# Performance work log

Hardware: AMD Instinct MI355X
Metric: run time of the kernel (lower is better)

The kernel has to match this reference:

```python
import jax, jax.numpy as jnp
import numpy as np

HEADS = 8
GROUPS = 8  # min(8, ch)
EPS = 1e-5


def group_norm(x, gamma, beta):
    # x: (B, C, H, W); normalize over (C/G, H, W) per group
    B, C, H, W = x.shape
    xg = x.reshape(B, GROUPS, C // GROUPS, H, W)
    mu = jnp.mean(xg, axis=(2, 3, 4), keepdims=True)
    var = jnp.var(xg, axis=(2, 3, 4), keepdims=True)
    xn = ((xg - mu) * jax.lax.rsqrt(var + EPS)).reshape(B, C, H, W)
    return xn * gamma[None, :, None, None] + beta[None, :, None, None]


def setup_inputs() -> dict:
    key = jax.random.key(0)
    k1, k2, k3 = jax.random.split(key, 3)
    B, C, H, W = 8, 512, 32, 32
    x = jax.random.normal(k1, (B, C, H, W), dtype=jnp.float32)
    gn_gamma = jnp.ones((C,), dtype=jnp.float32)
    gn_beta = jnp.zeros((C,), dtype=jnp.float32)
    # conv1x1 weights, torch shape (out,in,1,1) squeezed to (out,in)
    w_qkv = jax.random.normal(k2, (3 * C, C), dtype=jnp.float32) * (1.0 / np.sqrt(C))
    w_proj = jax.random.normal(k3, (C, C), dtype=jnp.float32) * (1.0 / np.sqrt(C))
    b_proj = jnp.zeros((C,), dtype=jnp.float32)
    return {"x": x, "gn_gamma": gn_gamma, "gn_beta": gn_beta,
            "w_qkv": w_qkv, "w_proj": w_proj, "b_proj": b_proj}


def reference(x, gn_gamma, gn_beta, w_qkv, w_proj, b_proj):
    B, C, H, W = x.shape
    hd = C // HEADS  # head_dim
    N = H * W
    xn = group_norm(x, gn_gamma, gn_beta)
    # 1x1 conv == channel matmul: (B,3C,H,W)
    qkv = jnp.einsum('oc,bchw->bohw', w_qkv, xn)
    q, k, v = jnp.split(qkv, 3, axis=1)

    def sh(t):  # (B,C,H,W) -> (B, heads, N, head_dim)
        return t.reshape(B, HEADS, hd, N).transpose(0, 1, 3, 2)

    q, k, v = sh(q), sh(k), sh(v)
    scale = hd ** -0.5
    attn = jax.nn.softmax(jnp.einsum('bhnd,bhmd->bhnm', q, k) * scale, axis=-1)
    out = jnp.einsum('bhnm,bhmd->bhnd', attn, v)  # (B,heads,N,hd)
    out = out.transpose(0, 1, 3, 2).reshape(B, C, H, W)
    proj = jnp.einsum('oc,bchw->bohw', w_proj, out) + b_proj[None, :, None, None]
    return x + proj
```

## Files before the change

kernel.cpp:

```cpp
#include <hip/hip_runtime.h>
#include <cstdint>


typedef __bf16 bf16_t;
typedef bf16_t bf16x8 __attribute__((ext_vector_type(8)));
typedef float f32x4 __attribute__((ext_vector_type(4)));

__device__ __forceinline__ uint16_t f2bf(float f) {
  uint32_t x = __builtin_bit_cast(uint32_t, f);
  x += 0x7FFFu + ((x >> 16) & 1u);
  return (uint16_t)(x >> 16);
}
__device__ __forceinline__ bf16x8 frag_ld(const uint16_t* p) {
  return __builtin_bit_cast(bf16x8, *(const uint4*)p);
}
__device__ __forceinline__ void gl_lds16(const uint16_t* g, uint16_t* l) {
  __builtin_amdgcn_global_load_lds(
      (const __attribute__((address_space(1))) uint32_t*)g,
      (__attribute__((address_space(3))) uint32_t*)l, 16, 0, 0);
}
#define MFMA16(a, b, c) __builtin_amdgcn_mfma_f32_16x16x32_bf16((a), (b), (c), 0, 0, 0)

__global__ __launch_bounds__(256) void prep_k(const float* __restrict__ wq,
                                              const float* __restrict__ wp,
                                              uint16_t* __restrict__ wqb,
                                              uint16_t* __restrict__ wpb,
                                              const float* __restrict__ x,
                                              float* __restrict__ stats) {
  __shared__ alignas(16) float r1[256];
  __shared__ alignas(16) float r2[256];
  int bx = blockIdx.x, t = threadIdx.x;
  if (bx < 512) {
    int idx = (bx * 256 + t) * 8;
    const float* s;
    uint16_t* d;
    if (idx < 786432) { s = wq + idx; d = wqb + idx; }
    else              { s = wp + (idx - 786432); d = wpb + (idx - 786432); }
    float4 a = *(const float4*)s;
    float4 b = *(const float4*)(s + 4);
    union { uint16_t u[8]; uint4 v; } o;
    o.u[0] = f2bf(a.x); o.u[1] = f2bf(a.y); o.u[2] = f2bf(a.z); o.u[3] = f2bf(a.w);
    o.u[4] = f2bf(b.x); o.u[5] = f2bf(b.y); o.u[6] = f2bf(b.z); o.u[7] = f2bf(b.w);
    *(uint4*)d = o.v;
    return;
  }
  int pg = bx - 512;
  const float4* p4 = (const float4*)(x + (size_t)(pg >> 2) * 65536 + (pg & 3) * 16384);
  float s1 = 0.f, s2 = 0.f;
  for (int i = t; i < 4096; i += 256) {
    float4 u = p4[i];
    s1 += u.x + u.y + u.z + u.w;
    s2 += u.x * u.x + u.y * u.y + u.z * u.z + u.w * u.w;
  }
  r1[t] = s1; r2[t] = s2; __syncthreads();
  for (int o = 128; o > 0; o >>= 1) {
    if (t < o) { r1[t] += r1[t + o]; r2[t] += r2[t + o]; }
    __syncthreads();
  }
  if (t == 0) { stats[pg * 2] = r1[0]; stats[pg * 2 + 1] = r2[0]; }
}

__global__ __launch_bounds__(256) void gn_apply_k(const float* __restrict__ x,
                                                  const float* __restrict__ gamma,
                                                  const float* __restrict__ beta,
                                                  const float* __restrict__ stats,
                                                  uint16_t* __restrict__ xn) {
  int nt = blockIdx.x, g = blockIdx.y, b = blockIdx.z;
  int n0 = nt * 64;
  int bg = b * 8 + g;
  float s1 = 0.f, s2 = 0.f;
#pragma unroll
  for (int p = 0; p < 4; p++) { s1 += stats[(bg * 4 + p) * 2]; s2 += stats[(bg * 4 + p) * 2 + 1]; }
  float mu   = s1 * (1.0f / 65536.0f);
  float var  = s2 * (1.0f / 65536.0f) - mu * mu;
  float rstd = rsqrtf(var + 1e-5f);
  __shared__ alignas(16) uint16_t tile[64][72];
  int t = threadIdx.x;
  {
    int c_loc = t >> 2;
    int nch = (t & 3) * 16;
    int c = g * 64 + c_loc;
    float gm = gamma[c], bt = beta[c];
    const float* src = x + (size_t)b * 524288 + (size_t)c * 1024 + n0 + nch;
#pragma unroll
    for (int hh = 0; hh < 2; hh++) {
      float4 u0 = *(const float4*)(src + hh * 8);
      float4 u1 = *(const float4*)(src + hh * 8 + 4);
      union { uint16_t u16[8]; uint4 v; } o;
      o.u16[0] = f2bf((u0.x - mu) * rstd * gm + bt);
      o.u16[1] = f2bf((u0.y - mu) * rstd * gm + bt);
      o.u16[2] = f2bf((u0.z - mu) * rstd * gm + bt);
      o.u16[3] = f2bf((u0.w - mu) * rstd * gm + bt);
      o.u16[4] = f2bf((u1.x - mu) * rstd * gm + bt);
      o.u16[5] = f2bf((u1.y - mu) * rstd * gm + bt);
      o.u16[6] = f2bf((u1.z - mu) * rstd * gm + bt);
      o.u16[7] = f2bf((u1.w - mu) * rstd * gm + bt);
      *(uint4*)&tile[c_loc][nch + hh * 8] = o.v;
    }
  }
  __syncthreads();
  {
    int n_loc = t >> 2;
    int c0 = (t & 3) * 16;
    union { uint16_t u16[16]; uint4 v[2]; } o;
#pragma unroll
    for (int j = 0; j < 16; j++) o.u16[j] = tile[c0 + j][n_loc];
    uint16_t* dst = xn + (size_t)b * 524288 + (size_t)(n0 + n_loc) * 512 + g * 64 + c0;
    *(uint4*)dst = o.v[0];
    *(uint4*)(dst + 8) = o.v[1];
  }
}

template <int MODE>
__device__ __forceinline__ void gemm_body(uint16_t* Sh,
                                          const uint16_t* Arow, const uint16_t* Brow,
                                          uint16_t* O0, uint16_t* O1,
                                          int b, int n0, int o0) {
  uint16_t* As = Sh;
  uint16_t* Bs = Sh + 8192;
  int t = threadIdx.x;
  int lane = t & 63, w = t >> 6;
  int qd = lane >> 4, l15 = lane & 15;
  int wm = w & 1, wn = w >> 1;

  const uint16_t* gA[4];
  const uint16_t* gB[4];
  uint16_t* lA[4];
  uint16_t* lB[4];
#pragma unroll
  for (int i = 0; i < 4; i++) {
    int p = i * 256 + t;
    int row = p >> 3, slot = p & 7, gc = slot ^ (row & 7);
    gA[i] = Arow + (size_t)row * 512 + gc * 8;
    gB[i] = Brow + (size_t)row * 512 + gc * 8;
    lA[i] = As + (size_t)(p - lane) * 8;
    lB[i] = Bs + (size_t)(p - lane) * 8;
  }

  f32x4 acc[4][4] = {};

  for (int k0 = 0; k0 < 512; k0 += 64) {
    __syncthreads();
#pragma unroll
    for (int i = 0; i < 4; i++) { gl_lds16(gA[i] + k0, lA[i]); gl_lds16(gB[i] + k0, lB[i]); }
    __syncthreads();

#pragma unroll
    for (int h = 0; h < 2; h++) {
      int slot = (h * 4 + qd) ^ (l15 & 7);
      bf16x8 af[4], bfr[4];
#pragma unroll
      for (int mt = 0; mt < 4; mt++)
        af[mt] = frag_ld(As + (wm * 64 + mt * 16 + l15) * 64 + slot * 8);
#pragma unroll
      for (int nt2 = 0; nt2 < 4; nt2++)
        bfr[nt2] = frag_ld(Bs + (wn * 64 + nt2 * 16 + l15) * 64 + slot * 8);
#pragma unroll
      for (int mt = 0; mt < 4; mt++)
#pragma unroll
        for (int nt2 = 0; nt2 < 4; nt2++)
          acc[mt][nt2] = MFMA16(af[mt], bfr[nt2], acc[mt][nt2]);
    }
  }

  __syncthreads();
  uint16_t* buf = Sh + w * 1152;
  float sc = 1.0f;
  uint16_t* gbase;
  size_t rstride;
  int coff;
  if constexpr (MODE == 0) {
    int oc = o0 + wn * 64;
    int hh;
    uint16_t* db;
    if (oc < 512) { db = O0; hh = oc >> 6; sc = 0.125f; }
    else          { db = O1; hh = (oc - 512) >> 6; }
    gbase = db + (size_t)(b * 8 + hh) * 65536 + (size_t)(n0 + wm * 64) * 64;
    rstride = 64;  coff = 0;
  } else {
    gbase = O0 + (size_t)b * 524288 + (size_t)(o0 + wm * 64) * 1024;
    rstride = 1024; coff = n0 + wn * 64;
  }
  int jrow = lane >> 3, joff = (lane & 7) * 8;
#pragma unroll
  for (int mt = 0; mt < 4; mt++) {
#pragma unroll
    for (int nt2 = 0; nt2 < 4; nt2++)
#pragma unroll
      for (int r = 0; r < 4; r++)
        buf[(qd * 4 + r) * 72 + nt2 * 16 + l15] = f2bf(acc[mt][nt2][r] * sc);
#pragma unroll
    for (int half = 0; half < 2; half++) {
      int row = jrow + half * 8;
      uint4 v = *(const uint4*)(buf + row * 72 + joff);
      *(uint4*)(gbase + (size_t)(mt * 16 + row) * rstride + coff + joff) = v;
    }
  }
}

__global__ __launch_bounds__(256) void gemm01_k(const uint16_t* __restrict__ xn,
                                                const uint16_t* __restrict__ wqb,
                                                uint16_t* __restrict__ qtw,
                                                uint16_t* __restrict__ ktw,
                                                uint16_t* __restrict__ vtw) {
  __shared__ alignas(16) uint16_t Sh[16384];
  int id = blockIdx.x;
  int lo = id & 7, hi = id >> 3;
  int o12 = hi % 12, b = hi / 12;
  int n0 = lo * 128;
  if (o12 < 8) {
    int o0 = o12 * 128;
    gemm_body<0>(Sh, xn + (size_t)b * 524288 + (size_t)n0 * 512,
                 wqb + (size_t)o0 * 512, qtw, ktw, b, n0, o0);
  } else {
    int o0 = (o12 - 8) * 128;
    gemm_body<1>(Sh, wqb + (size_t)(1024 + o0) * 512,
                 xn + (size_t)b * 524288 + (size_t)n0 * 512, vtw, nullptr, b, n0, o0);
  }
}

__global__ __launch_bounds__(256) void gemm2_k(const uint16_t* __restrict__ wpb,
                                               const uint16_t* __restrict__ otw,
                                               const float* __restrict__ xres,
                                               const float* __restrict__ biasf,
                                               float* __restrict__ out) {
  __shared__ alignas(16) uint16_t As[2][8192];
  __shared__ alignas(16) uint16_t Bs[2][8192];
  int id = blockIdx.x;
  int lo = id & 7, hi = id >> 3;
  int o0 = (hi & 3) * 128, b = hi >> 2, n0 = lo * 128;
  const uint16_t* Arow = wpb + (size_t)o0 * 512;
  const uint16_t* Brow = otw + (size_t)b * 524288 + (size_t)n0 * 512;

  int t = threadIdx.x, lane = t & 63, w = t >> 6;
  int qd = lane >> 4, l15 = lane & 15;
  int wm = w & 1, wn = w >> 1;

  const uint16_t* gA[4];
  const uint16_t* gB[4];
  int lofs[4];
#pragma unroll
  for (int i = 0; i < 4; i++) {
    int p = i * 256 + t;
    int row = p >> 3, slot = p & 7, gc = slot ^ (row & 7);
    gA[i] = Arow + (size_t)row * 512 + gc * 8;
    gB[i] = Brow + (size_t)row * 512 + gc * 8;
    lofs[i] = (p - lane) * 8;
  }

  f32x4 acc[4][4] = {};
#pragma unroll
  for (int i = 0; i < 4; i++) { gl_lds16(gA[i], &As[0][lofs[i]]); gl_lds16(gB[i], &Bs[0][lofs[i]]); }
  __syncthreads();

  for (int kt = 0; kt < 8; kt++) {
    int cur = kt & 1, nxt = cur ^ 1;
    if (kt < 7) {
      int k0 = (kt + 1) * 64;
#pragma unroll
      for (int i = 0; i < 4; i++) { gl_lds16(gA[i] + k0, &As[nxt][lofs[i]]); gl_lds16(gB[i] + k0, &Bs[nxt][lofs[i]]); }
    }
#pragma unroll
    for (int h = 0; h < 2; h++) {
      int slot = (h * 4 + qd) ^ (l15 & 7);
      bf16x8 af[4], bfr[4];
#pragma unroll
      for (int mt = 0; mt < 4; mt++)
        af[mt] = frag_ld(&As[cur][(wm * 64 + mt * 16 + l15) * 64 + slot * 8]);
#pragma unroll
      for (int nt2 = 0; nt2 < 4; nt2++)
        bfr[nt2] = frag_ld(&Bs[cur][(wn * 64 + nt2 * 16 + l15) * 64 + slot * 8]);
#pragma unroll
      for (int mt = 0; mt < 4; mt++)
#pragma unroll
        for (int nt2 = 0; nt2 < 4; nt2++)
          acc[mt][nt2] = MFMA16(af[mt], bfr[nt2], acc[mt][nt2]);
    }
    __syncthreads();
  }

#pragma unroll
  for (int mt = 0; mt < 4; mt++) {
    int row = wm * 64 + mt * 16 + qd * 4;
#pragma unroll
    for (int nt2 = 0; nt2 < 4; nt2++) {
      int col = wn * 64 + nt2 * 16 + l15;
#pragma unroll
      for (int r = 0; r < 4; r++) {
        int orow = o0 + row + r, n = n0 + col;
        size_t idx = (size_t)b * 524288 + (size_t)orow * 1024 + n;
        out[idx] = xres[idx] + biasf[orow] + acc[mt][nt2][r];
      }
    }
  }
}

__global__ __launch_bounds__(256) void attn_k(const uint16_t* __restrict__ qt,
                                              const uint16_t* __restrict__ ktp,
                                              const uint16_t* __restrict__ vtp,
                                              uint16_t* __restrict__ ot) {
  int bh = blockIdx.x;
  int b = bh >> 3, h = bh & 7;
  int n0 = blockIdx.y * 128;
  const uint16_t* qbase = qt + (size_t)bh * 65536;
  const uint16_t* kbase = ktp + (size_t)bh * 65536;
  const uint16_t* vbase = vtp + (size_t)b * 524288 + (size_t)h * 65536;

  __shared__ alignas(16) uint16_t Ks[2][64 * 64];
  __shared__ alignas(16) uint16_t Vs[2][64 * 64];
  __shared__ alignas(16) uint16_t Ps[128 * 72];

  int t = threadIdx.x, lane = t & 63, w = t >> 6;
  int qd = lane >> 4, l15 = lane & 15;

  bf16x8 qf[2][2];
#pragma unroll
  for (int rs = 0; rs < 2; rs++) {
    const uint16_t* qp = qbase + (size_t)(n0 + w * 32 + rs * 16 + l15) * 64 + qd * 8;
    qf[rs][0] = frag_ld(qp);
    qf[rs][1] = frag_ld(qp + 32);
  }

  int p1 = t, p2 = t + 256;
  int r1 = p1 >> 3, gc1 = (p1 & 7) ^ (r1 & 7);
  int r2 = p2 >> 3, gc2 = (p2 & 7) ^ (r2 & 7);
  const uint16_t* gK1 = kbase + (size_t)r1 * 64 + gc1 * 8;
  const uint16_t* gK2 = kbase + (size_t)r2 * 64 + gc2 * 8;
  const uint16_t* gV1 = vbase + (size_t)r1 * 1024 + gc1 * 8;
  const uint16_t* gV2 = vbase + (size_t)r2 * 1024 + gc2 * 8;
  int lo1 = (p1 - lane) * 8;
  int lo2 = (p2 - lane) * 8;

  f32x4 oaccT[2][4] = {};
  float lsum[2] = {0.f, 0.f};

  gl_lds16(gK1, &Ks[0][lo1]);
  gl_lds16(gK2, &Ks[0][lo2]);
  gl_lds16(gV1, &Vs[0][lo1]);
  gl_lds16(gV2, &Vs[0][lo2]);
  __syncthreads();

  for (int it = 0; it < 16; it++) {
    int cur = it & 1, nxt = cur ^ 1;
    if (it < 15) {
      int m0 = (it + 1) * 64;
      gl_lds16(gK1 + (size_t)m0 * 64, &Ks[nxt][lo1]);
      gl_lds16(gK2 + (size_t)m0 * 64, &Ks[nxt][lo2]);
      gl_lds16(gV1 + m0, &Vs[nxt][lo1]);
      gl_lds16(gV2 + m0, &Vs[nxt][lo2]);
    }
    const uint16_t* Kc = Ks[cur];
    const uint16_t* Vc = Vs[cur];

    f32x4 sacc[2][4] = {};
#pragma unroll
    for (int mt = 0; mt < 4; mt++) {
      int row = mt * 16 + l15;
      int s0 = qd ^ (l15 & 7);
      bf16x8 kf0 = frag_ld(Kc + (size_t)row * 64 + s0 * 8);
      bf16x8 kf1 = frag_ld(Kc + (size_t)row * 64 + (s0 ^ 4) * 8);
#pragma unroll
      for (int rs = 0; rs < 2; rs++) {
        sacc[rs][mt] = MFMA16(kf0, qf[rs][0], sacc[rs][mt]);
        sacc[rs][mt] = MFMA16(kf1, qf[rs][1], sacc[rs][mt]);
      }
    }

#pragma unroll
    for (int rs = 0; rs < 2; rs++)
#pragma unroll
      for (int mt = 0; mt < 4; mt++) {
        union { uint16_t u[4]; uint2 v; } pk;
        float psum = 0.f;
#pragma unroll
        for (int r = 0; r < 4; r++) {
          float p = __expf(sacc[rs][mt][r]);
          psum += p;
          pk.u[r] = (uint16_t)(__builtin_bit_cast(uint32_t, p) >> 16);
        }
        lsum[rs] += psum;
        *(uint2*)(Ps + (size_t)(w * 32 + rs * 16 + l15) * 72 + mt * 16 + qd * 4) = pk.v;
      }

    bf16x8 pf[2][2];
#pragma unroll
    for (int rs = 0; rs < 2; rs++)
#pragma unroll
      for (int ks = 0; ks < 2; ks++)
        pf[rs][ks] = frag_ld(Ps + (size_t)(w * 32 + rs * 16 + l15) * 72 + ks * 32 + qd * 8);
#pragma unroll
    for (int dt = 0; dt < 4; dt++)
#pragma unroll
      for (int ks = 0; ks < 2; ks++) {
        int row = dt * 16 + l15;
        int slot = (ks * 4 + qd) ^ (l15 & 7);
        bf16x8 vf = frag_ld(Vc + (size_t)row * 64 + slot * 8);
#pragma unroll
        for (int rs = 0; rs < 2; rs++)
          oaccT[rs][dt] = MFMA16(vf, pf[rs][ks], oaccT[rs][dt]);
      }

    __syncthreads();
  }

#pragma unroll
  for (int rs = 0; rs < 2; rs++) {
    float s = lsum[rs];
    s += __shfl_xor(s, 16);
    s += __shfl_xor(s, 32);
    float rinv = 1.0f / s;
    int n = n0 + w * 32 + rs * 16 + l15;
    uint16_t* orow = ot + (size_t)b * 524288 + (size_t)n * 512 + h * 64;
#pragma unroll
    for (int dt = 0; dt < 4; dt++) {
      union { uint16_t u[4]; uint2 v; } pk;
#pragma unroll
      for (int r = 0; r < 4; r++) pk.u[r] = f2bf(oaccT[rs][dt][r] * rinv);
      *(uint2*)(orow + dt * 16 + qd * 4) = pk.v;
    }
  }
}

extern "C" void kernel_launch(void* const* d_in, const int* in_sizes, int n_in,
                              void* d_out, int out_size, void* d_ws, size_t ws_size,
                              hipStream_t stream) {
  (void)in_sizes; (void)n_in; (void)out_size; (void)ws_size;
  const float* xf   = (const float*)d_in[0];
  const float* gamf = (const float*)d_in[1];
  const float* betf = (const float*)d_in[2];
  const float* wqf  = (const float*)d_in[3];
  const float* wpf  = (const float*)d_in[4];
  const float* bprf = (const float*)d_in[5];
  float* out = (float*)d_out;

  uint16_t* base = (uint16_t*)d_ws;
  float* stats   = (float*)base;
  uint16_t* wqb  = base + 1024;
  uint16_t* wpb  = wqb + 786432;
  uint16_t* xn   = wpb + 262144;
  uint16_t* qtw  = xn  + 4194304;
  uint16_t* ktw  = qtw + 4194304;
  uint16_t* vtw  = ktw + 4194304;
  uint16_t* otw  = xn;

  prep_k<<<768, 256, 0, stream>>>(wqf, wpf, wqb, wpb, xf, stats);
  gn_apply_k<<<dim3(16, 8, 8), 256, 0, stream>>>(xf, gamf, betf, stats, xn);
  gemm01_k<<<768, 256, 0, stream>>>(xn, wqb, qtw, ktw, vtw);
  attn_k<<<dim3(64, 8), 256, 0, stream>>>(qtw, ktw, vtw, otw);
  gemm2_k<<<256, 256, 0, stream>>>(wpb, otw, xf, bprf, out);
}
```

Before: 147.7 us.

## Halve attention block to 2 waves with 64 query rows each, move prefetch after QK

```diff
diff --git a/kernel.cpp b/kernel.cpp
--- a/kernel.cpp
+++ b/kernel.cpp
@@ -295,7 +295,7 @@
   }
 }
 
-__global__ __launch_bounds__(256) void attn_k(const uint16_t* __restrict__ qt,
+__global__ __launch_bounds__(128) void attn_k(const uint16_t* __restrict__ qt,
                                               const uint16_t* __restrict__ ktp,
                                               const uint16_t* __restrict__ vtp,
                                               uint16_t* __restrict__ ot) {
@@ -306,53 +306,46 @@
   const uint16_t* kbase = ktp + (size_t)bh * 65536;
   const uint16_t* vbase = vtp + (size_t)b * 524288 + (size_t)h * 65536;
 
-  __shared__ alignas(16) uint16_t Ks[2][64 * 64];
-  __shared__ alignas(16) uint16_t Vs[2][64 * 64];
+  __shared__ alignas(16) uint16_t Ks[2][4096];
+  __shared__ alignas(16) uint16_t Vs[2][4096];
   __shared__ alignas(16) uint16_t Ps[128 * 72];
 
   int t = threadIdx.x, lane = t & 63, w = t >> 6;
   int qd = lane >> 4, l15 = lane & 15;
 
-  bf16x8 qf[2][2];
-#pragma unroll
-  for (int rs = 0; rs < 2; rs++) {
-    const uint16_t* qp = qbase + (size_t)(n0 + w * 32 + rs * 16 + l15) * 64 + qd * 8;
+  bf16x8 qf[4][2];
+#pragma unroll
+  for (int rs = 0; rs < 4; rs++) {
+    const uint16_t* qp = qbase + (size_t)(n0 + w * 64 + rs * 16 + l15) * 64 + qd * 8;
     qf[rs][0] = frag_ld(qp);
     qf[rs][1] = frag_ld(qp + 32);
   }
 
-  int p1 = t, p2 = t + 256;
-  int r1 = p1 >> 3, gc1 = (p1 & 7) ^ (r1 & 7);
-  int r2 = p2 >> 3, gc2 = (p2 & 7) ^ (r2 & 7);
-  const uint16_t* gK1 = kbase + (size_t)r1 * 64 + gc1 * 8;
-  const uint16_t* gK2 = kbase + (size_t)r2 * 64 + gc2 * 8;
-  const uint16_t* gV1 = vbase + (size_t)r1 * 1024 + gc1 * 8;
-  const uint16_t* gV2 = vbase + (size_t)r2 * 1024 + gc2 * 8;
-  int lo1 = (p1 - lane) * 8;
-  int lo2 = (p2 - lane) * 8;
-
-  f32x4 oaccT[2][4] = {};
-  float lsum[2] = {0.f, 0.f};
-
-  gl_lds16(gK1, &Ks[0][lo1]);
-  gl_lds16(gK2, &Ks[0][lo2]);
-  gl_lds16(gV1, &Vs[0][lo1]);
-  gl_lds16(gV2, &Vs[0][lo2]);
+  const uint16_t* gK[4];
+  const uint16_t* gV[4];
+  int lofs[4];
+#pragma unroll
+  for (int i = 0; i < 4; i++) {
+    int p = i * 128 + t;
+    int row = p >> 3, slot = p & 7, gc = slot ^ (row & 7);
+    gK[i] = kbase + (size_t)row * 64 + gc * 8;
+    gV[i] = vbase + (size_t)row * 1024 + gc * 8;
+    lofs[i] = (p - lane) * 8;
+  }
+
+  f32x4 oaccT[4][4] = {};
+  float lsum[4] = {0.f, 0.f, 0.f, 0.f};
+
+#pragma unroll
+  for (int i = 0; i < 4; i++) { gl_lds16(gK[i], &Ks[0][lofs[i]]); gl_lds16(gV[i], &Vs[0][lofs[i]]); }
   __syncthreads();
 
   for (int it = 0; it < 16; it++) {
     int cur = it & 1, nxt = cur ^ 1;
-    if (it < 15) {
-      int m0 = (it + 1) * 64;
-      gl_lds16(gK1 + (size_t)m0 * 64, &Ks[nxt][lo1]);
-      gl_lds16(gK2 + (size_t)m0 * 64, &Ks[nxt][lo2]);
-      gl_lds16(gV1 + m0, &Vs[nxt][lo1]);
-      gl_lds16(gV2 + m0, &Vs[nxt][lo2]);
-    }
     const uint16_t* Kc = Ks[cur];
     const uint16_t* Vc = Vs[cur];
 
-    f32x4 sacc[2][4] = {};
+    f32x4 sacc[4][4];
 #pragma unroll
     for (int mt = 0; mt < 4; mt++) {
       int row = mt * 16 + l15;
@@ -360,14 +353,24 @@
       bf16x8 kf0 = frag_ld(Kc + (size_t)row * 64 + s0 * 8);
       bf16x8 kf1 = frag_ld(Kc + (size_t)row * 64 + (s0 ^ 4) * 8);
 #pragma unroll
-      for (int rs = 0; rs < 2; rs++) {
-        sacc[rs][mt] = MFMA16(kf0, qf[rs][0], sacc[rs][mt]);
-        sacc[rs][mt] = MFMA16(kf1, qf[rs][1], sacc[rs][mt]);
+      for (int rs = 0; rs < 4; rs++) {
+        f32x4 z = {};
+        z = MFMA16(kf0, qf[rs][0], z);
+        sacc[rs][mt] = MFMA16(kf1, qf[rs][1], z);
       }
     }
 
-#pragma unroll
-    for (int rs = 0; rs < 2; rs++)
+    if (it < 15) {
+      int m0 = (it + 1) * 64;
+#pragma unroll
+      for (int i = 0; i < 4; i++) {
+        gl_lds16(gK[i] + (size_t)m0 * 64, &Ks[nxt][lofs[i]]);
+        gl_lds16(gV[i] + m0, &Vs[nxt][lofs[i]]);
+      }
+    }
+
+#pragma unroll
+    for (int rs = 0; rs < 4; rs++)
 #pragma unroll
       for (int mt = 0; mt < 4; mt++) {
         union { uint16_t u[4]; uint2 v; } pk;
@@ -379,15 +382,15 @@
           pk.u[r] = (uint16_t)(__builtin_bit_cast(uint32_t, p) >> 16);
         }
         lsum[rs] += psum;
-        *(uint2*)(Ps + (size_t)(w * 32 + rs * 16 + l15) * 72 + mt * 16 + qd * 4) = pk.v;
+        *(uint2*)(Ps + (size_t)(w * 64 + rs * 16 + l15) * 72 + mt * 16 + qd * 4) = pk.v;
       }
 
-    bf16x8 pf[2][2];
-#pragma unroll
-    for (int rs = 0; rs < 2; rs++)
+    bf16x8 pf[4][2];
+#pragma unroll
+    for (int rs = 0; rs < 4; rs++)
 #pragma unroll
       for (int ks = 0; ks < 2; ks++)
-        pf[rs][ks] = frag_ld(Ps + (size_t)(w * 32 + rs * 16 + l15) * 72 + ks * 32 + qd * 8);
+        pf[rs][ks] = frag_ld(Ps + (size_t)(w * 64 + rs * 16 + l15) * 72 + ks * 32 + qd * 8);
 #pragma unroll
     for (int dt = 0; dt < 4; dt++)
 #pragma unroll
@@ -396,7 +399,7 @@
         int slot = (ks * 4 + qd) ^ (l15 & 7);
         bf16x8 vf = frag_ld(Vc + (size_t)row * 64 + slot * 8);
 #pragma unroll
-        for (int rs = 0; rs < 2; rs++)
+        for (int rs = 0; rs < 4; rs++)
           oaccT[rs][dt] = MFMA16(vf, pf[rs][ks], oaccT[rs][dt]);
       }
 
@@ -404,12 +407,12 @@
   }
 
 #pragma unroll
-  for (int rs = 0; rs < 2; rs++) {
+  for (int rs = 0; rs < 4; rs++) {
     float s = lsum[rs];
     s += __shfl_xor(s, 16);
     s += __shfl_xor(s, 32);
     float rinv = 1.0f / s;
-    int n = n0 + w * 32 + rs * 16 + l15;
+    int n = n0 + w * 64 + rs * 16 + l15;
     uint16_t* orow = ot + (size_t)b * 524288 + (size_t)n * 512 + h * 64;
 #pragma unroll
     for (int dt = 0; dt < 4; dt++) {
@@ -446,6 +449,6 @@
   prep_k<<<768, 256, 0, stream>>>(wqf, wpf, wqb, wpb, xf, stats);
   gn_apply_k<<<dim3(16, 8, 8), 256, 0, stream>>>(xf, gamf, betf, stats, xn);
   gemm01_k<<<768, 256, 0, stream>>>(xn, wqb, qtw, ktw, vtw);
-  attn_k<<<dim3(64, 8), 256, 0, stream>>>(qtw, ktw, vtw, otw);
+  attn_k<<<dim3(64, 8), 128, 0, stream>>>(qtw, ktw, vtw, otw);
   gemm2_k<<<256, 256, 0, stream>>>(wpb, otw, xf, bprf, out);
 }
```

After: 152.7 us. 1.03x slower.
